# Performance work log

Hardware: AMD Instinct MI355X
Metric: run time of the kernel (lower is better)

## Reference

```python
import jax, jax.numpy as jnp
import numpy as np

B, C, H, W = 8, 1024, 56, 56
NBINS = 256          # torch.histc(bins=256, min=0, max=1)
T_THRESH = 0.9       # EKLM entropy-ratio threshold
NUM_CLASSES = 30


def setup_inputs() -> dict:
    key = jax.random.key(0)
    k1, k2 = jax.random.split(key)
    x = jax.random.uniform(k1, (B, C, H, W), dtype=jnp.float32)
    w_fc = jax.random.normal(k2, (C, NUM_CLASSES), dtype=jnp.float32) * 0.02
    return {"x": x, "w_fc": w_fc}


def _integral_hist(x):
    """One fused pass replacing the per-region torch.histc calls.
    Returns per-(h,w)-cell histograms [H,W,256] and their 2D inclusive
    prefix sum padded to [H+1,W+1,256] so any rectangle histogram is 4 lookups.
    Matches torch.histc semantics: values outside [0,1] ignored, v==1 -> last bin."""
    valid = (x >= 0.0) & (x <= 1.0)
    q = jnp.clip(jnp.floor(x * NBINS), 0, NBINS - 1).astype(jnp.int32)
    q = jnp.where(valid, q, NBINS)  # out-of-range -> extra bin, dropped below
    hh = jnp.broadcast_to(jnp.arange(H)[None, None, :, None], x.shape)
    ww = jnp.broadcast_to(jnp.arange(W)[None, None, None, :], x.shape)
    cell = jnp.zeros((H, W, NBINS + 1), jnp.float32).at[hh, ww, q].add(1.0)[..., :NBINS]
    integ = jnp.cumsum(jnp.cumsum(cell, axis=0), axis=1)
    integ = jnp.pad(integ, ((1, 0), (1, 0), (0, 0)))  # [H+1, W+1, 256]
    return cell, integ


def _entropy_of_hist(h):
    p = h / jnp.sum(h)
    return -jnp.sum(p * jnp.log2(p + 1e-9))


def _region_entropy(integ, xs, xd, ys, yd):
    # histogram of x[:, :, xs:xd, ys:yd] via integral-histogram lookups
    h = integ[xd, yd] - integ[xs, yd] - integ[xd, ys] + integ[xs, ys]
    return _entropy_of_hist(h)


def eklm(x):
    """Entropy-based Key Localization Method (xs fixed to 0, as in source)."""
    cell, integ = _integral_hist(x)
    # compute_entropy_for_each_y: entropy of each [:, :, 0:1, y:y+1] column cell
    col_hists = cell[0]  # [W, 256]
    p = col_hists / jnp.sum(col_hists, axis=1, keepdims=True)
    ent_y = -jnp.sum(p * jnp.log2(p + 1e-9), axis=1)
    ys0 = jnp.argmax(ent_y).astype(jnp.int32)
    total_ent = _region_entropy(integ, 0, H, 0, W)

    def ent(xd, ys, yd):
        return _region_entropy(integ, 0, xd, ys, yd)

    def cond(state):
        xd, ys, yd, Ts, done = state
        return (Ts < T_THRESH) & (~done)

    def body(state):
        xd, ys, yd, Ts, done = state
        e_cur = ent(xd, ys, yd)
        # greedy priority identical to source: grow xd, else shrink ys, else grow yd
        c1 = (xd + 1 < H) & (ent(xd + 1, ys, yd) > e_cur)
        c2 = (~c1) & (ys - 1 >= 0) & (ent(xd, jnp.maximum(ys - 1, 0), yd) > e_cur)
        c3 = (~c1) & (~c2) & (yd + 1 < W) & (ent(xd, ys, jnp.minimum(yd + 1, W)) > e_cur)
        xd_n = jnp.where(c1, xd + 1, xd)
        ys_n = jnp.where(c2, ys - 1, ys)
        yd_n = jnp.where(c3, yd + 1, yd)
        done_n = ~(c1 | c2 | c3)
        Ts_n = ent(xd_n, ys_n, yd_n) / total_ent
        return (xd_n, ys_n, yd_n, Ts_n, done_n)

    xd0 = jnp.int32(1)
    yd0 = ys0 + jnp.int32(1)
    Ts0 = ent(xd0, ys0, yd0) / total_ent
    xd, ys, yd, _, _ = jax.lax.while_loop(
        cond, body, (xd0, ys0, yd0, Ts0, jnp.bool_(False)))
    return jnp.int32(0), xd, ys, yd


def reference(x, w_fc):
    xs, xd, ys, yd = eklm(x)
    # crop the located key region (mask form for static shapes), mean-pool, classify
    row = jnp.arange(H)
    col = jnp.arange(W)
    mask = ((row[:, None] >= xs) & (row[:, None] < xd)
            & (col[None, :] >= ys) & (col[None, :] < yd)).astype(x.dtype)
    area = jnp.maximum(jnp.sum(mask), 1.0)
    pooled = jnp.einsum('bchw,hw->bc', x, mask) / area  # [B, C]
    return pooled @ w_fc  # [B, NUM_CLASSES]
```

## Files before the change

### kernel.cpp

```cpp
#include <hip/hip_runtime.h>
#include <math.h>

#define BB 8
#define CC 1024
#define HH 56
#define WW 56
#define NB 256
#define NCLS 30
#define BC (BB * CC)
#define PLANE (HH * WW)
#define NWORD (NB / 2)
#define CELLW (HH * WW * NWORD)
#define SLICES 16
#define WSPLIT 2
#define WHALF (WW / WSPLIT)
#define PL_PER_SLICE (BC / SLICES)
#define HTHREADS 256
#define VEC4_PER_BLOCK (PL_PER_SLICE * WHALF / 4)
#define LH_WORDS (WHALF * NWORD)

template <bool ATOMIC_FLUSH>
__global__ __launch_bounds__(HTHREADS) void hist_kernel(const float* __restrict__ x,
                                                        unsigned* __restrict__ dst) {
    __shared__ unsigned lh[LH_WORDS];
    const int tid = threadIdx.x;
    const int bid = blockIdx.x;
    const int whalf = bid & (WSPLIT - 1);
    const int hs = bid / WSPLIT;
    const int h = hs % HH;
    const int slice = hs / HH;

    for (int i = tid; i < LH_WORDS; i += HTHREADS) lh[i] = 0u;
    __syncthreads();

    const float* __restrict__ xb =
        x + (size_t)(slice * PL_PER_SLICE) * PLANE + h * WW + whalf * WHALF;

#pragma unroll
    for (int it = 0; it < VEC4_PER_BLOCK / HTHREADS; ++it) {
        const int j = it * HTHREADS + tid;
        const int bcl = j / 7;
        const int wq = j - bcl * 7;
        const float4 v = *(const float4*)(xb + (size_t)bcl * PLANE + wq * 4);
        const float vv[4] = {v.x, v.y, v.z, v.w};
#pragma unroll
        for (int e = 0; e < 4; ++e) {
            const float f = vv[e];
            if (f >= 0.f && f <= 1.f) {
                int bin = (int)(f * 256.f);
                if (bin > 255) bin = 255;
                const int wl = wq * 4 + e;
                atomicAdd(&lh[wl * NWORD + (bin >> 1)], 1u << ((bin & 1) << 4));
            }
        }
    }
    __syncthreads();

    if (ATOMIC_FLUSH) {
        unsigned* g = dst + ((size_t)h * WW + whalf * WHALF) * NWORD;
        for (int i = tid; i < LH_WORDS; i += HTHREADS) {
            const unsigned v = lh[i];
            if (v) atomicAdd(&g[i], v);
        }
    } else {
        unsigned* g = dst + ((size_t)hs * WW + whalf * WHALF) * NWORD;
        for (int i = tid; i < LH_WORDS; i += HTHREADS) g[i] = lh[i];
    }
}

__global__ void reduce_kernel(const unsigned* __restrict__ ps,
                              unsigned* __restrict__ hist) {
    const int idx = blockIdx.x * 256 + threadIdx.x;
    unsigned s = 0;
#pragma unroll
    for (int sl = 0; sl < SLICES; ++sl) s += ps[(size_t)sl * CELLW + idx];
    ((uint2*)hist)[idx] = make_uint2(s & 0xffffu, s >> 16);
}

__global__ void unpack_kernel(const unsigned* __restrict__ hp,
                              unsigned* __restrict__ hist) {
    const int idx = blockIdx.x * 256 + threadIdx.x;
    const unsigned s = hp[idx];
    ((uint2*)hist)[idx] = make_uint2(s & 0xffffu, s >> 16);
}

__global__ void cumw_kernel(unsigned* __restrict__ hist) {
    const int h = blockIdx.x, b = threadIdx.x;
    unsigned* base = hist + (size_t)h * WW * NB + b;
    unsigned v[WW];
#pragma unroll
    for (int w = 0; w < WW; ++w) v[w] = base[(size_t)w * NB];
    unsigned c = 0;
#pragma unroll
    for (int w = 0; w < WW; ++w) { c += v[w]; base[(size_t)w * NB] = c; }
}

__global__ void cumh_kernel(unsigned* __restrict__ hist) {
    const int w = blockIdx.x, b = threadIdx.x;
    unsigned* base = hist + (size_t)w * NB + b;
    unsigned v[HH];
#pragma unroll
    for (int h = 0; h < HH; ++h) v[h] = base[(size_t)h * WW * NB];
    unsigned c = 0;
#pragma unroll
    for (int h = 0; h < HH; ++h) { c += v[h]; base[(size_t)h * WW * NB] = c; }
}

__device__ __forceinline__ float wave_sum(float v) {
#pragma unroll
    for (int off = 32; off > 0; off >>= 1) v += __shfl_xor(v, off);
    return v;
}

__device__ __forceinline__ float ilook(const unsigned* __restrict__ integ,
                                       int a, int b, int bin) {
    return (a == 0 || b == 0)
               ? 0.f
               : (float)integ[((size_t)((a - 1) * WW + (b - 1))) * NB + bin];
}

__device__ float region_ent(const unsigned* __restrict__ integ, int lane,
                            int xd, int ys, int yd) {
    float hb[4];
    float hs = 0.f;
#pragma unroll
    for (int k = 0; k < 4; k++) {
        const int bin = lane + 64 * k;
        const float hv = ilook(integ, xd, yd, bin) - ilook(integ, xd, ys, bin);
        hb[k] = hv;
        hs += hv;
    }
    hs = wave_sum(hs);
    float e = 0.f;
#pragma unroll
    for (int k = 0; k < 4; k++) {
        const float p = hb[k] / hs;
        e += p * log2f(p + 1e-9f);
    }
    return -wave_sum(e);
}

__global__ __launch_bounds__(1024) void decide_kernel(const unsigned* __restrict__ integ,
                                                      int* __restrict__ region) {
    __shared__ float ent_s[WW];
    const int tid = threadIdx.x;
    const int lane = tid & 63;
    const int wv = tid >> 6;

    for (int w = wv; w < WW; w += 16) {
        float hb[4], hs = 0.f;
#pragma unroll
        for (int k = 0; k < 4; k++) {
            const int bin = lane + 64 * k;
            const float a = (float)integ[(size_t)w * NB + bin];
            const float b = w ? (float)integ[(size_t)(w - 1) * NB + bin] : 0.f;
            hb[k] = a - b;
            hs += hb[k];
        }
        hs = wave_sum(hs);
        float e = 0.f;
#pragma unroll
        for (int k = 0; k < 4; k++) {
            const float p = hb[k] / hs;
            e += p * log2f(p + 1e-9f);
        }
        e = -wave_sum(e);
        if (lane == 0) ent_s[w] = e;
    }
    __syncthreads();
    if (wv != 0) return;

    float best = -3.0e38f;
    int bestw = 0;
    for (int w = 0; w < WW; ++w) {
        const float e = ent_s[w];
        if (e > best) { best = e; bestw = w; }
    }

    const float total_ent = region_ent(integ, lane, HH, 0, WW);

    int xd = 1, ys = bestw, yd = bestw + 1;
    float Ts = region_ent(integ, lane, xd, ys, yd) / total_ent;
    bool done = false;
    int iter = 0;
    while (Ts < 0.9f && !done && iter < 1000) {
        iter++;
        const float e_cur = region_ent(integ, lane, xd, ys, yd);
        const int ysm = (ys - 1 < 0) ? 0 : ys - 1;
        const int ydp = (yd + 1 > WW) ? WW : yd + 1;
        const bool c1 = (xd + 1 < HH) && (region_ent(integ, lane, xd + 1, ys, yd) > e_cur);
        const bool c2 = !c1 && (ys - 1 >= 0) && (region_ent(integ, lane, xd, ysm, yd) > e_cur);
        const bool c3 = !c1 && !c2 && (yd + 1 < WW) && (region_ent(integ, lane, xd, ys, ydp) > e_cur);
        if (c1) xd = xd + 1;
        else if (c2) ys = ys - 1;
        else if (c3) yd = yd + 1;
        done = !(c1 || c2 || c3);
        Ts = region_ent(integ, lane, xd, ys, yd) / total_ent;
    }

    if (lane == 0) {
        region[0] = xd;
        region[1] = ys;
        region[2] = yd;
    }
}

__global__ void pool_kernel(const float* __restrict__ x,
                            const int* __restrict__ region,
                            float* __restrict__ pooled) {
    const int bc = blockIdx.x;
    const int xd = region[0], ys = region[1], yd = region[2];
    const int Wd = yd - ys;
    const int n = xd * Wd;
    const float area = fmaxf((float)n, 1.f);
    const float* plane = x + (size_t)bc * PLANE;
    float s = 0.f;
    for (int j = threadIdx.x; j < n; j += 64) {
        const int r = j / Wd;
        const int cc = ys + (j - r * Wd);
        s += plane[r * WW + cc];
    }
#pragma unroll
    for (int off = 32; off > 0; off >>= 1) s += __shfl_xor(s, off);
    if (threadIdx.x == 0) pooled[bc] = s / area;
}

__global__ __launch_bounds__(256) void fc_kernel(const float* __restrict__ pooled,
                                                 const float* __restrict__ wfc,
                                                 float* __restrict__ out) {
    __shared__ float red[240];
    const int b = blockIdx.x;
    const int t = threadIdx.x;
    if (t < 240) {
        const int chunk = t / NCLS;
        const int n = t - chunk * NCLS;
        const float* pv = pooled + b * CC + chunk * 128;
        const float* wv = wfc + (size_t)(chunk * 128) * NCLS + n;
        float a0 = 0.f, a1 = 0.f, a2 = 0.f, a3 = 0.f;
        for (int c = 0; c < 128; c += 4) {
            a0 += pv[c + 0] * wv[(c + 0) * NCLS];
            a1 += pv[c + 1] * wv[(c + 1) * NCLS];
            a2 += pv[c + 2] * wv[(c + 2) * NCLS];
            a3 += pv[c + 3] * wv[(c + 3) * NCLS];
        }
        red[t] = (a0 + a1) + (a2 + a3);
    }
    __syncthreads();
    if (t < NCLS) {
        float s = 0.f;
#pragma unroll
        for (int ch = 0; ch < 8; ++ch) s += red[ch * NCLS + t];
        out[b * NCLS + t] = s;
    }
}

extern "C" void kernel_launch(void* const* d_in, const int* in_sizes, int n_in,
                              void* d_out, int out_size, void* d_ws, size_t ws_size,
                              hipStream_t stream) {
    const float* x = (const float*)d_in[0];
    const float* wfc = (const float*)d_in[1];
    float* out = (float*)d_out;

    unsigned char* ws = (unsigned char*)d_ws;
    const size_t ps_bytes = (size_t)SLICES * CELLW * 4;
    const size_t hist_bytes = (size_t)CELLW * 8;
    const size_t needA = ps_bytes + hist_bytes + 4096 + (size_t)BC * 4;

    if (ws_size >= needA) {
        unsigned* ps = (unsigned*)ws;
        unsigned* hist = (unsigned*)(ws + ps_bytes);
        int* region = (int*)(ws + ps_bytes + hist_bytes);
        float* pooled = (float*)(ws + ps_bytes + hist_bytes + 4096);

        hist_kernel<false><<<HH * WSPLIT * SLICES, HTHREADS, 0, stream>>>(x, ps);
        reduce_kernel<<<CELLW / 256, 256, 0, stream>>>(ps, hist);
        cumw_kernel<<<HH, NB, 0, stream>>>(hist);
        cumh_kernel<<<WW, NB, 0, stream>>>(hist);
        decide_kernel<<<1, 1024, 0, stream>>>(hist, region);
        pool_kernel<<<BC, 64, 0, stream>>>(x, region, pooled);
        fc_kernel<<<BB, 256, 0, stream>>>(pooled, wfc, out);
    } else {
        unsigned* hp = (unsigned*)ws;
        unsigned* hist = (unsigned*)(ws + (size_t)CELLW * 4);
        int* region = (int*)(ws + (size_t)CELLW * 4 + hist_bytes);
        float* pooled = (float*)(ws + (size_t)CELLW * 4 + hist_bytes + 4096);

        hipMemsetAsync(hp, 0, (size_t)CELLW * 4, stream);
        hist_kernel<true><<<HH * WSPLIT * SLICES, HTHREADS, 0, stream>>>(x, hp);
        unpack_kernel<<<CELLW / 256, 256, 0, stream>>>(hp, hist);
        cumw_kernel<<<HH, NB, 0, stream>>>(hist);
        cumh_kernel<<<WW, NB, 0, stream>>>(hist);
        decide_kernel<<<1, 1024, 0, stream>>>(hist, region);
        pool_kernel<<<BC, 64, 0, stream>>>(x, region, pooled);
        fc_kernel<<<BB, 256, 0, stream>>>(pooled, wfc, out);
    }
}
```

Baseline: 188.8 us.

## Fuse slice reduction and 2D prefix sums into one per-bin shared-memory kernel

Partial histograms are now written bin-word-major, so one block per bin can sum the slices, unpack the 16-bit halves and run both row and column prefix scans in shared memory. This replaces the separate reduce, cumw and cumh kernels and their global round trips. The hist kernel also pads the shared histogram pitch to 129 to spread LDS bank use and double-buffers its float4 loads to hide load latency. The cost is serial scans run by only 56 threads per block and strided global writes into the integral layout.

```diff
diff --git a/kernel.cpp b/kernel.cpp
--- a/kernel.cpp
+++ b/kernel.cpp
@@ -9,20 +9,23 @@
 #define NCLS 30
 #define BC (BB * CC)
 #define PLANE (HH * WW)
+#define CELLS (HH * WW)
 #define NWORD (NB / 2)
-#define CELLW (HH * WW * NWORD)
 #define SLICES 16
 #define WSPLIT 2
 #define WHALF (WW / WSPLIT)
 #define PL_PER_SLICE (BC / SLICES)
 #define HTHREADS 256
 #define VEC4_PER_BLOCK (PL_PER_SLICE * WHALF / 4)
-#define LH_WORDS (WHALF * NWORD)
+#define HIST_ITERS (VEC4_PER_BLOCK / HTHREADS)
+#define LH_PITCH 129
+#define LH_TOT (WHALF * LH_PITCH)
+#define FLUSH_N (NWORD * WHALF)
 
 template <bool ATOMIC_FLUSH>
 __global__ __launch_bounds__(HTHREADS) void hist_kernel(const float* __restrict__ x,
                                                         unsigned* __restrict__ dst) {
-    __shared__ unsigned lh[LH_WORDS];
+    __shared__ unsigned lh[LH_TOT];
     const int tid = threadIdx.x;
     const int bid = blockIdx.x;
     const int whalf = bid & (WSPLIT - 1);
@@ -30,80 +33,92 @@
     const int h = hs % HH;
     const int slice = hs / HH;
 
-    for (int i = tid; i < LH_WORDS; i += HTHREADS) lh[i] = 0u;
+    for (int i = tid; i < LH_TOT; i += HTHREADS) lh[i] = 0u;
     __syncthreads();
 
     const float* __restrict__ xb =
         x + (size_t)(slice * PL_PER_SLICE) * PLANE + h * WW + whalf * WHALF;
 
-#pragma unroll
-    for (int it = 0; it < VEC4_PER_BLOCK / HTHREADS; ++it) {
+    auto ldv = [&](int it) {
         const int j = it * HTHREADS + tid;
         const int bcl = j / 7;
         const int wq = j - bcl * 7;
-        const float4 v = *(const float4*)(xb + (size_t)bcl * PLANE + wq * 4);
-        const float vv[4] = {v.x, v.y, v.z, v.w};
+        return *(const float4*)(xb + (size_t)bcl * PLANE + wq * 4);
+    };
+    auto wqof = [&](int it) {
+        const int j = it * HTHREADS + tid;
+        return j - (j / 7) * 7;
+    };
+
+    float4 b0 = ldv(0);
+    float4 b1 = ldv(1);
+#pragma unroll
+    for (int it = 0; it < HIST_ITERS; ++it) {
+        const float4 cur = b0;
+        b0 = b1;
+        if (it < HIST_ITERS - 2) b1 = ldv(it + 2);
+        const int wl0 = wqof(it) * 4;
+        const float vv[4] = {cur.x, cur.y, cur.z, cur.w};
 #pragma unroll
         for (int e = 0; e < 4; ++e) {
             const float f = vv[e];
             if (f >= 0.f && f <= 1.f) {
                 int bin = (int)(f * 256.f);
                 if (bin > 255) bin = 255;
-                const int wl = wq * 4 + e;
-                atomicAdd(&lh[wl * NWORD + (bin >> 1)], 1u << ((bin & 1) << 4));
+                atomicAdd(&lh[(wl0 + e) * LH_PITCH + (bin >> 1)],
+                          1u << ((bin & 1) << 4));
             }
         }
     }
     __syncthreads();
 
-    if (ATOMIC_FLUSH) {
-        unsigned* g = dst + ((size_t)h * WW + whalf * WHALF) * NWORD;
-        for (int i = tid; i < LH_WORDS; i += HTHREADS) {
-            const unsigned v = lh[i];
-            if (v) atomicAdd(&g[i], v);
-        }
-    } else {
-        unsigned* g = dst + ((size_t)hs * WW + whalf * WHALF) * NWORD;
-        for (int i = tid; i < LH_WORDS; i += HTHREADS) g[i] = lh[i];
-    }
-}
-
-__global__ void reduce_kernel(const unsigned* __restrict__ ps,
-                              unsigned* __restrict__ hist) {
-    const int idx = blockIdx.x * 256 + threadIdx.x;
-    unsigned s = 0;
-#pragma unroll
-    for (int sl = 0; sl < SLICES; ++sl) s += ps[(size_t)sl * CELLW + idx];
-    ((uint2*)hist)[idx] = make_uint2(s & 0xffffu, s >> 16);
-}
-
-__global__ void unpack_kernel(const unsigned* __restrict__ hp,
-                              unsigned* __restrict__ hist) {
-    const int idx = blockIdx.x * 256 + threadIdx.x;
-    const unsigned s = hp[idx];
-    ((uint2*)hist)[idx] = make_uint2(s & 0xffffu, s >> 16);
-}
-
-__global__ void cumw_kernel(unsigned* __restrict__ hist) {
-    const int h = blockIdx.x, b = threadIdx.x;
-    unsigned* base = hist + (size_t)h * WW * NB + b;
-    unsigned v[WW];
-#pragma unroll
-    for (int w = 0; w < WW; ++w) v[w] = base[(size_t)w * NB];
-    unsigned c = 0;
-#pragma unroll
-    for (int w = 0; w < WW; ++w) { c += v[w]; base[(size_t)w * NB] = c; }
-}
-
-__global__ void cumh_kernel(unsigned* __restrict__ hist) {
-    const int w = blockIdx.x, b = threadIdx.x;
-    unsigned* base = hist + (size_t)w * NB + b;
-    unsigned v[HH];
-#pragma unroll
-    for (int h = 0; h < HH; ++h) v[h] = base[(size_t)h * WW * NB];
-    unsigned c = 0;
-#pragma unroll
-    for (int h = 0; h < HH; ++h) { c += v[h]; base[(size_t)h * WW * NB] = c; }
+    for (int i = tid; i < FLUSH_N; i += HTHREADS) {
+        const int word = i / WHALF;
+        const int wl = i - word * WHALF;
+        const unsigned v = lh[wl * LH_PITCH + word];
+        const int cell = h * WW + whalf * WHALF + wl;
+        if (ATOMIC_FLUSH) {
+            if (v) atomicAdd(&dst[(size_t)word * CELLS + cell], v);
+        } else {
+            dst[((size_t)word * SLICES + slice) * CELLS + cell] = v;
+        }
+    }
+}
+
+template <int NSL>
+__global__ __launch_bounds__(256) void cum2d_kernel(const unsigned* __restrict__ ps,
+                                                    unsigned* __restrict__ integ) {
+    __shared__ unsigned acc[CELLS];
+    const int bin = blockIdx.x;
+    const int word = bin >> 1;
+    const int sh = (bin & 1) << 4;
+    const unsigned* __restrict__ base = ps + (size_t)word * NSL * CELLS;
+
+    for (int c = threadIdx.x; c < CELLS; c += 256) {
+        unsigned s = 0;
+#pragma unroll
+        for (int sl = 0; sl < NSL; ++sl) s += base[(size_t)sl * CELLS + c];
+        acc[c] = (s >> sh) & 0xffffu;
+    }
+    __syncthreads();
+
+    if (threadIdx.x < HH) {
+        unsigned run = 0;
+        const int rb = threadIdx.x * WW;
+        for (int w = 0; w < WW; ++w) { run += acc[rb + w]; acc[rb + w] = run; }
+    }
+    __syncthreads();
+    if (threadIdx.x < WW) {
+        unsigned run = 0;
+        for (int h = 0; h < HH; ++h) {
+            run += acc[h * WW + threadIdx.x];
+            acc[h * WW + threadIdx.x] = run;
+        }
+    }
+    __syncthreads();
+
+    for (int c = threadIdx.x; c < CELLS; c += 256)
+        integ[(size_t)c * NB + bin] = acc[c];
 }
 
 __device__ __forceinline__ float wave_sum(float v) {
@@ -262,35 +277,32 @@
     float* out = (float*)d_out;
 
     unsigned char* ws = (unsigned char*)d_ws;
-    const size_t ps_bytes = (size_t)SLICES * CELLW * 4;
-    const size_t hist_bytes = (size_t)CELLW * 8;
-    const size_t needA = ps_bytes + hist_bytes + 4096 + (size_t)BC * 4;
+    const size_t ps_bytes = (size_t)NWORD * SLICES * CELLS * 4;
+    const size_t integ_bytes = (size_t)CELLS * NB * 4;
+    const size_t needA = ps_bytes + integ_bytes + 4096 + (size_t)BC * 4;
 
     if (ws_size >= needA) {
         unsigned* ps = (unsigned*)ws;
-        unsigned* hist = (unsigned*)(ws + ps_bytes);
-        int* region = (int*)(ws + ps_bytes + hist_bytes);
-        float* pooled = (float*)(ws + ps_bytes + hist_bytes + 4096);
+        unsigned* integ = (unsigned*)(ws + ps_bytes);
+        int* region = (int*)(ws + ps_bytes + integ_bytes);
+        float* pooled = (float*)(ws + ps_bytes + integ_bytes + 4096);
 
         hist_kernel<false><<<HH * WSPLIT * SLICES, HTHREADS, 0, stream>>>(x, ps);
-        reduce_kernel<<<CELLW / 256, 256, 0, stream>>>(ps, hist);
-        cumw_kernel<<<HH, NB, 0, stream>>>(hist);
-        cumh_kernel<<<WW, NB, 0, stream>>>(hist);
-        decide_kernel<<<1, 1024, 0, stream>>>(hist, region);
+        cum2d_kernel<SLICES><<<NB, 256, 0, stream>>>(ps, integ);
+        decide_kernel<<<1, 1024, 0, stream>>>(integ, region);
         pool_kernel<<<BC, 64, 0, stream>>>(x, region, pooled);
         fc_kernel<<<BB, 256, 0, stream>>>(pooled, wfc, out);
     } else {
         unsigned* hp = (unsigned*)ws;
-        unsigned* hist = (unsigned*)(ws + (size_t)CELLW * 4);
-        int* region = (int*)(ws + (size_t)CELLW * 4 + hist_bytes);
-        float* pooled = (float*)(ws + (size_t)CELLW * 4 + hist_bytes + 4096);
-
-        hipMemsetAsync(hp, 0, (size_t)CELLW * 4, stream);
+        const size_t hp_bytes = (size_t)NWORD * CELLS * 4;
+        unsigned* integ = (unsigned*)(ws + hp_bytes);
+        int* region = (int*)(ws + hp_bytes + integ_bytes);
+        float* pooled = (float*)(ws + hp_bytes + integ_bytes + 4096);
+
+        hipMemsetAsync(hp, 0, hp_bytes, stream);
         hist_kernel<true><<<HH * WSPLIT * SLICES, HTHREADS, 0, stream>>>(x, hp);
-        unpack_kernel<<<CELLW / 256, 256, 0, stream>>>(hp, hist);
-        cumw_kernel<<<HH, NB, 0, stream>>>(hist);
-        cumh_kernel<<<WW, NB, 0, stream>>>(hist);
-        decide_kernel<<<1, 1024, 0, stream>>>(hist, region);
+        cum2d_kernel<1><<<NB, 256, 0, stream>>>(hp, integ);
+        decide_kernel<<<1, 1024, 0, stream>>>(integ, region);
         pool_kernel<<<BC, 64, 0, stream>>>(x, region, pooled);
         fc_kernel<<<BB, 256, 0, stream>>>(pooled, wfc, out);
     }
```

Result: slower. 217.0 us (+14.9%).
